# Performance work log

Hardware: AMD Instinct MI355X
Metric: run time of the kernel (lower is better)

## Reference

```python
import jax, jax.numpy as jnp
import numpy as np

B, T, S = 16, 512, 512
V, E, H = 10000, 512, 1024
L, K, MAXLEN = 6, 3, 1024
PAD_VAL = 1.0  # torch code pads conv input with tgt_pad_idx as a float value


def setup_inputs() -> dict:
    key = jax.random.key(0)
    ks = jax.random.split(key, 12)
    g = lambda k, shape: (jax.random.normal(k, shape, jnp.float32) * 0.02)
    return {
        "tgt": jax.random.randint(ks[0], (B, T), 0, V),
        "encoder_conved": jax.random.normal(ks[1], (B, S, E), jnp.float32),
        "encoder_combined": jax.random.normal(ks[2], (B, S, E), jnp.float32),
        "tok_emb": g(ks[3], (V, E)),
        "pos_emb": g(ks[4], (MAXLEN, E)),
        "emb2hid_w": g(ks[5], (E, H)), "emb2hid_b": jnp.zeros((H,), jnp.float32),
        "hid2emb_w": g(ks[6], (H, E)), "hid2emb_b": jnp.zeros((E,), jnp.float32),
        "attn_hid2emb_w": g(ks[7], (H, E)), "attn_hid2emb_b": jnp.zeros((E,), jnp.float32),
        "attn_emb2hid_w": g(ks[8], (E, H)), "attn_emb2hid_b": jnp.zeros((H,), jnp.float32),
        "fc_out_w": g(ks[9], (E, V)), "fc_out_b": jnp.zeros((V,), jnp.float32),
        "conv_w": g(ks[10], (L, 2 * H, H, K)),  # torch Conv1d weight: [out, in, k]
        "conv_b": jnp.zeros((L, 2 * H), jnp.float32),
    }


def reference(tgt, encoder_conved, encoder_combined, tok_emb, pos_emb,
              emb2hid_w, emb2hid_b, hid2emb_w, hid2emb_b,
              attn_hid2emb_w, attn_hid2emb_b, attn_emb2hid_w, attn_emb2hid_b,
              fc_out_w, fc_out_b, conv_w, conv_b):
    scale = jnp.float32(np.sqrt(0.5))
    b, t = tgt.shape
    h = emb2hid_w.shape[1]
    k = conv_w.shape[-1]

    # embeddings (dropout=0 -> identity)
    embedded = tok_emb[tgt] + pos_emb[jnp.arange(t)][None, :, :]   # [B,T,E]
    conv_input = (embedded @ emb2hid_w + emb2hid_b).transpose(0, 2, 1)  # [B,H,T]

    attention = None
    for l in range(conv_w.shape[0]):
        # causal left-pad with the (float) pad-index value, as in the torch code
        pad = jnp.full((b, h, k - 1), PAD_VAL, conv_input.dtype)
        x = jnp.concatenate([pad, conv_input], axis=2)              # [B,H,T+K-1]
        conved = jax.lax.conv_general_dilated(
            x, conv_w[l], window_strides=(1,), padding='VALID',
            dimension_numbers=('NCH', 'OIH', 'NCH')) + conv_b[l][None, :, None]  # [B,2H,T]
        a, g = jnp.split(conved, 2, axis=1)
        conved = a * jax.nn.sigmoid(g)                              # GLU -> [B,H,T]

        # single-head attention over encoder states
        conved_emb = conved.transpose(0, 2, 1) @ attn_hid2emb_w + attn_hid2emb_b  # [B,T,E]
        combined = (conved_emb + embedded) * scale
        energy = jnp.einsum('bte,bse->bts', combined, encoder_conved)
        attention = jax.nn.softmax(energy, axis=2)                  # [B,T,S]
        attended = jnp.einsum('bts,bse->bte', attention, encoder_combined)
        attended = attended @ attn_emb2hid_w + attn_emb2hid_b       # [B,T,H]
        conved = (conved + attended.transpose(0, 2, 1)) * scale     # [B,H,T]

        conv_input = (conved + conv_input) * scale                  # scaled residual

    conved = conv_input.transpose(0, 2, 1) @ hid2emb_w + hid2emb_b  # [B,T,E]
    output = conved @ fc_out_w + fc_out_b                           # [B,T,V]
    return output, attention
```

## Files before the change

kernel.cpp:

```cpp
#include <hip/hip_runtime.h>
#include <hip/hip_bf16.h>

typedef __attribute__((ext_vector_type(4))) float f32x4;
typedef __attribute__((ext_vector_type(8))) short short8;

#define DEVFN __device__ __forceinline__

static constexpr int Bn = 16, Tn = 512, Sn = 512, Vn = 10000, En = 512, Hn = 1024, Ln = 6;
static constexpr int Mn = Bn * Tn;
static constexpr int TP = Tn + 2;
static constexpr float kScale = 0.70710678118654752440f;

DEVFN float bf2f(__hip_bfloat16 x) { return __bfloat162float(x); }
DEVFN __hip_bfloat16 f2bf(float x) { return __float2bfloat16(x); }

struct bf16x4 { __hip_bfloat16 x, y, z, w; };

DEVFN void gload_lds16(const short* g, short* l) {
    __builtin_amdgcn_global_load_lds((const __attribute__((address_space(1))) void*)g,
                                     (__attribute__((address_space(3))) void*)l, 16, 0, 0);
}


__global__ void padfill_kernel(__hip_bfloat16* p) {
    p[threadIdx.x] = f2bf(1.0f);
}

__global__ void padrows_kernel(__hip_bfloat16* convinP) {
    int row = blockIdx.x;
    long base = ((long)(row >> 1) * TP + (row & 1)) * Hn;
    int e = threadIdx.x * 4;
    bf16x4 v{f2bf(1.f), f2bf(1.f), f2bf(1.f), f2bf(1.f)};
    *(bf16x4*)(convinP + base + e) = v;
}

__global__ void embed_kernel(const int* __restrict__ tgt, const float* __restrict__ tok,
                             const float* __restrict__ pos, const float* __restrict__ bah,
                             __hip_bfloat16* __restrict__ out, __hip_bfloat16* __restrict__ outA) {
    int row = blockIdx.x;
    int t = row & (Tn - 1);
    int v = tgt[row];
    const float* tr = tok + (long)v * En;
    const float* pr = pos + (long)t * En;
    int e = threadIdx.x * 4;
    float4 a = *(const float4*)(tr + e);
    float4 b = *(const float4*)(pr + e);
    float4 bb = *(const float4*)(bah + e);
    bf16x4 o{f2bf(a.x + b.x), f2bf(a.y + b.y), f2bf(a.z + b.z), f2bf(a.w + b.w)};
    *(bf16x4*)(out + (long)row * En + e) = o;
    bf16x4 oa{f2bf(kScale * (a.x + b.x + bb.x)), f2bf(kScale * (a.y + b.y + bb.y)),
              f2bf(kScale * (a.z + b.z + bb.z)), f2bf(kScale * (a.w + b.w + bb.w))};
    *(bf16x4*)(outA + (long)row * En + e) = oa;
}

__global__ void transpose_f32_bf16(const float* __restrict__ src, __hip_bfloat16* __restrict__ dst,
                                   int R, int C, long sZi, long sZo) {
    __shared__ float tile[32][33];
    src += (long)blockIdx.z * sZi;
    dst += (long)blockIdx.z * sZo;
    int c0 = blockIdx.x * 32, r0 = blockIdx.y * 32;
    for (int i = threadIdx.y; i < 32; i += 8) {
        int r = r0 + i, c = c0 + threadIdx.x;
        tile[i][threadIdx.x] = (r < R && c < C) ? src[(long)r * C + c] : 0.f;
    }
    __syncthreads();
    for (int i = threadIdx.y; i < 32; i += 8) {
        int c = c0 + i, r = r0 + threadIdx.x;
        if (c < C && r < R) dst[(long)c * R + r] = f2bf(tile[threadIdx.x][i]);
    }
}

__global__ void convert_bf16_kernel(const float* __restrict__ src, __hip_bfloat16* __restrict__ dst,
                                    long n4) {
    long i = (long)blockIdx.x * blockDim.x + threadIdx.x;
    if (i >= n4) return;
    long j = i * 4;
    float4 v = *(const float4*)(src + j);
    bf16x4 o{f2bf(v.x), f2bf(v.y), f2bf(v.z), f2bf(v.w)};
    *(bf16x4*)(dst + j) = o;
}

__global__ __launch_bounds__(256) void wpack2_kernel(const float* __restrict__ convw,
                                                     __hip_bfloat16* __restrict__ wp, int l) {
    __shared__ float row[3 * Hn];
    int c = blockIdx.x;
    int grp = c >> 5, w = c & 31;
    int o = (w < 16) ? grp * 16 + w : Hn + grp * 16 + (w - 16);
    const float* src = convw + ((long)(l * 2 * Hn + o)) * (Hn * 3);
#pragma unroll
    for (int j = 0; j < 3; ++j) {
        int idx = (j * 256 + threadIdx.x) * 4;
        *(float4*)&row[idx] = *(const float4*)(src + idx);
    }
    __syncthreads();
    __hip_bfloat16* dst = wp + (long)c * (3 * Hn);
#pragma unroll
    for (int j = 0; j < 3; ++j) {
        int kk = (j * 256 + threadIdx.x) * 4;
        int tap = kk >> 10;
        int i = kk & (Hn - 1);
        bf16x4 v{f2bf(row[i * 3 + tap]), f2bf(row[(i + 1) * 3 + tap]),
                 f2bf(row[(i + 2) * 3 + tap]), f2bf(row[(i + 3) * 3 + tap])};
        *(bf16x4*)(dst + kk) = v;
    }
}

__global__ __launch_bounds__(256) void softmax_kernel(const float* __restrict__ energy,
                                                      float* __restrict__ attn_f32,
                                                      __hip_bfloat16* __restrict__ attn_bf) {
    int row = blockIdx.x;
    const float* e = energy + (long)row * Sn;
    int tid = threadIdx.x;
    float v0 = e[tid], v1 = e[tid + 256];
    float m = fmaxf(v0, v1);
    for (int off = 32; off; off >>= 1) m = fmaxf(m, __shfl_xor(m, off));
    __shared__ float redm[4];
    __shared__ float reds[4];
    int lane = tid & 63, w = tid >> 6;
    if (lane == 0) redm[w] = m;
    __syncthreads();
    m = fmaxf(fmaxf(redm[0], redm[1]), fmaxf(redm[2], redm[3]));
    float x0 = __expf(v0 - m), x1 = __expf(v1 - m);
    float s = x0 + x1;
    for (int off = 32; off; off >>= 1) s += __shfl_xor(s, off);
    if (lane == 0) reds[w] = s;
    __syncthreads();
    s = reds[0] + reds[1] + reds[2] + reds[3];
    float inv = 1.f / s;
    long base = (long)row * Sn;
    if (attn_f32) {
        attn_f32[base + tid] = x0 * inv;
        attn_f32[base + tid + 256] = x1 * inv;
    }
    attn_bf[base + tid] = f2bf(x0 * inv);
    attn_bf[base + tid + 256] = f2bf(x1 * inv);
}

template <int EPI, bool OUTF32, bool NBOUND>
__global__ __launch_bounds__(256) void gemm_bf16(
    const __hip_bfloat16* __restrict__ A, const __hip_bfloat16* __restrict__ Bw,
    const float* __restrict__ bias, void* __restrict__ Cout,
    const __hip_bfloat16* __restrict__ R1, const __hip_bfloat16* __restrict__ R2,
    const float* __restrict__ R1f, const __hip_bfloat16* __restrict__ padrow,
    int M, int N, int K, long aZ, long bZ, long cZ, long r1Z, float s1, float s2) {
    __shared__ alignas(16) short As[2][128 * 32];
    __shared__ alignas(16) short Bs[2][128 * 32];
    const int tid = threadIdx.x;
    const int lane = tid & 63;
    const int wid = tid >> 6;
    const int wr = wid >> 1, wc = wid & 1;
    const int m0 = blockIdx.y * 128, n0 = blockIdx.x * 128;
    const short* Ag = (const short*)A + (long)blockIdx.z * aZ;
    const short* Bg = (const short*)Bw + (long)blockIdx.z * bZ;
    const short* pad = (const short*)padrow;

    f32x4 acc[4][4] = {};

    const int rc = tid >> 2;
    const int k8 = (tid & 3) * 8;

    auto stage = [&](int buf, int k0) {
#pragma unroll
        for (int j = 0; j < 2; ++j) {
            int r = rc + j * 64;
            const short* asrc = Ag + (long)(m0 + r) * K + k0 + k8;
            gload_lds16(asrc, &As[buf][r * 32 + k8]);
            int n = n0 + r;
            const short* bsrc = (NBOUND && n >= N) ? (pad + k8) : (Bg + (long)n * K + k0 + k8);
            gload_lds16(bsrc, &Bs[buf][r * 32 + k8]);
        }
    };

    const int rsel = lane & 15, hi = (lane >> 4) * 8;

    stage(0, 0);
    const int NT = K >> 5;
    for (int t = 0; t < NT; ++t) {
        const int cur = t & 1;
        if (t + 1 < NT) {
            stage(cur ^ 1, (t + 1) * 32);
            asm volatile("s_waitcnt vmcnt(4)" ::: "memory");
        } else {
            asm volatile("s_waitcnt vmcnt(0)" ::: "memory");
        }
        __builtin_amdgcn_s_barrier();
        __builtin_amdgcn_sched_barrier(0);
        short8 af[4], bg[4];
#pragma unroll
        for (int mi = 0; mi < 4; ++mi)
            af[mi] = *(const short8*)&As[cur][(wr * 64 + mi * 16 + rsel) * 32 + hi];
#pragma unroll
        for (int ni = 0; ni < 4; ++ni)
            bg[ni] = *(const short8*)&Bs[cur][(wc * 64 + ni * 16 + rsel) * 32 + hi];
        __builtin_amdgcn_s_setprio(1);
#pragma unroll
        for (int mi = 0; mi < 4; ++mi)
#pragma unroll
            for (int ni = 0; ni < 4; ++ni)
                acc[mi][ni] = __builtin_amdgcn_mfma_f32_16x16x32_bf16(af[mi], bg[ni], acc[mi][ni], 0, 0, 0);
        __builtin_amdgcn_s_setprio(0);
        __builtin_amdgcn_s_barrier();
        __builtin_amdgcn_sched_barrier(0);
    }

    const int rg = (lane >> 4) * 4;
    float* Cf = (float*)Cout + (long)blockIdx.z * cZ;
    __hip_bfloat16* Cb = (__hip_bfloat16*)Cout + (long)blockIdx.z * cZ;
    const __hip_bfloat16* R1z = R1 + (long)blockIdx.z * r1Z;
    const __hip_bfloat16* R2z = R2 + (long)blockIdx.z * cZ;
    const float* R1fz = R1f + (long)blockIdx.z * r1Z;
#pragma unroll
    for (int ni = 0; ni < 4; ++ni) {
        int col = n0 + wc * 64 + ni * 16 + rsel;
        if (NBOUND && col >= N) continue;
        float bi = (EPI != 3 && bias) ? bias[col] : 0.f;
#pragma unroll
        for (int mi = 0; mi < 4; ++mi) {
            int row = m0 + wr * 64 + mi * 16 + rg;
            f32x4 v = acc[mi][ni];
#pragma unroll
            for (int q = 0; q < 4; ++q) {
                long idx = (long)(row + q) * N + col;
                float x;
                if (EPI == 3) x = v[q] * s1 + R1fz[idx];
                else {
                    x = v[q] + bi;
                    if (EPI >= 1) x = (x + bf2f(R1z[idx])) * s1;
                    if (EPI >= 2) x = (x + bf2f(R2z[idx])) * s2;
                }
                if (OUTF32) Cf[idx] = x;
                else Cb[idx] = f2bf(x);
            }
        }
    }
}

template <int EPI, bool OUTF32>
__global__ __launch_bounds__(256) void gemm64(
    const __hip_bfloat16* __restrict__ A, const __hip_bfloat16* __restrict__ Bw,
    const float* __restrict__ bias, void* __restrict__ Cout,
    const __hip_bfloat16* __restrict__ R1, const __hip_bfloat16* __restrict__ R2,
    const float* __restrict__ R1f,
    int N, int K, long aZ, long bZ, long cZ, long r1Z, float s1, float s2) {
    __shared__ alignas(16) short As[2][64 * 32];
    __shared__ alignas(16) short Bs[2][128 * 32];
    const int tid = threadIdx.x;
    const int lane = tid & 63;
    const int wid = tid >> 6;
    const int m0 = blockIdx.y * 64, n0 = blockIdx.x * 128;
    const short* Ag = (const short*)A + (long)blockIdx.z * aZ;
    const short* Bg = (const short*)Bw + (long)blockIdx.z * bZ;

    f32x4 acc[4][2] = {};

    const int rc = tid >> 2;
    const int k8 = (tid & 3) * 8;

    auto stage = [&](int buf, int k0) {
        gload_lds16(Ag + (long)(m0 + rc) * K + k0 + k8, &As[buf][rc * 32 + k8]);
#pragma unroll
        for (int j = 0; j < 2; ++j) {
            int r = j * 64 + rc;
            gload_lds16(Bg + (long)(n0 + r) * K + k0 + k8, &Bs[buf][r * 32 + k8]);
        }
    };

    const int rsel = lane & 15, hi = (lane >> 4) * 8;

    stage(0, 0);
    const int NT = K >> 5;
    for (int t = 0; t < NT; ++t) {
        const int cur = t & 1;
        if (t + 1 < NT) {
            stage(cur ^ 1, (t + 1) * 32);
            asm volatile("s_waitcnt vmcnt(3)" ::: "memory");
        } else {
            asm volatile("s_waitcnt vmcnt(0)" ::: "memory");
        }
        __builtin_amdgcn_s_barrier();
        __builtin_amdgcn_sched_barrier(0);
        short8 af[4], bg[2];
#pragma unroll
        for (int mi = 0; mi < 4; ++mi)
            af[mi] = *(const short8*)&As[cur][(mi * 16 + rsel) * 32 + hi];
#pragma unroll
        for (int ni = 0; ni < 2; ++ni)
            bg[ni] = *(const short8*)&Bs[cur][(wid * 32 + ni * 16 + rsel) * 32 + hi];
        __builtin_amdgcn_s_setprio(1);
#pragma unroll
        for (int mi = 0; mi < 4; ++mi)
#pragma unroll
            for (int ni = 0; ni < 2; ++ni)
                acc[mi][ni] = __builtin_amdgcn_mfma_f32_16x16x32_bf16(af[mi], bg[ni], acc[mi][ni], 0, 0, 0);
        __builtin_amdgcn_s_setprio(0);
        __builtin_amdgcn_s_barrier();
        __builtin_amdgcn_sched_barrier(0);
    }

    const int rg = (lane >> 4) * 4;
    float* Cf = (float*)Cout + (long)blockIdx.z * cZ;
    __hip_bfloat16* Cb = (__hip_bfloat16*)Cout + (long)blockIdx.z * cZ;
    const __hip_bfloat16* R1z = R1 + (long)blockIdx.z * r1Z;
    const __hip_bfloat16* R2z = R2 + (long)blockIdx.z * cZ;
    const float* R1fz = R1f + (long)blockIdx.z * r1Z;
#pragma unroll
    for (int ni = 0; ni < 2; ++ni) {
        int col = n0 + wid * 32 + ni * 16 + rsel;
        float bi = (EPI != 3 && bias) ? bias[col] : 0.f;
#pragma unroll
        for (int mi = 0; mi < 4; ++mi) {
            int row = m0 + mi * 16 + rg;
            f32x4 v = acc[mi][ni];
#pragma unroll
            for (int q = 0; q < 4; ++q) {
                long idx = (long)(row + q) * N + col;
                float x;
                if (EPI == 3) x = v[q] * s1 + R1fz[idx];
                else {
                    x = v[q] + bi;
                    if (EPI >= 1) x = (x + bf2f(R1z[idx])) * s1;
                    if (EPI >= 2) x = (x + bf2f(R2z[idx])) * s2;
                }
                if (OUTF32) Cf[idx] = x;
                else Cb[idx] = f2bf(x);
            }
        }
    }
}

__global__ __launch_bounds__(512) void conv_glu_kernel(
    const __hip_bfloat16* __restrict__ Ain,
    const __hip_bfloat16* __restrict__ Bw,
    const float* __restrict__ bias, __hip_bfloat16* __restrict__ Cout,
    const __hip_bfloat16* __restrict__ padrow) {
    __shared__ alignas(16) short As[2][384 * 32];
    __shared__ alignas(16) short Bs[2][3 * 256 * 32];
    const int tid = threadIdx.x;
    const int lane = tid & 63;
    const int wid = tid >> 6;
    const int wr = wid >> 2, wc = wid & 3;
    const int n0 = blockIdx.x * 256, m0 = blockIdx.y * 256;
    const short* Ag = (const short*)Ain;
    const short* Bg = (const short*)Bw;
    const short* pad = (const short*)padrow;
    const int p0 = (m0 >> 9) * TP + 2 + (m0 & 511);

    f32x4 acc[8][4] = {};

    const int srow = tid >> 2;
    const int skey = (tid >> 3) & 3;
    const int scol = ((tid & 3) ^ skey) * 8;
    const int sdst = tid * 8;

    auto stageA = [&](int buf, int kt) {
        const int k0 = kt * 32;
#pragma unroll
        for (int j = 0; j < 3; ++j) {
            int prow = p0 - 128 + j * 128 + srow;
            const short* src = (prow >= 0) ? (Ag + (long)prow * Hn + k0 + scol) : (pad + scol);
            gload_lds16(src, &As[buf][j * 4096 + sdst]);
        }
    };
    auto stageB = [&](int buf, int kt) {
        const int k0 = kt * 32;
#pragma unroll
        for (int tap = 0; tap < 3; ++tap)
#pragma unroll
            for (int j = 0; j < 2; ++j) {
                int row = j * 128 + srow;
                const short* src = Bg + (long)(n0 + row) * 3072 + tap * 1024 + k0 + scol;
                gload_lds16(src, &Bs[buf][tap * 8192 + j * 4096 + sdst]);
            }
    };

    const int rsel = lane & 15, hi = (lane >> 4) * 8;

    stageA(0, 0); stageB(0, 0);
    for (int t = 0; t < 32; ++t) {
        const int cur = t & 1;
        if (t + 1 < 32) {
            stageA(cur ^ 1, t + 1); stageB(cur ^ 1, t + 1);
            asm volatile("s_waitcnt vmcnt(9)" ::: "memory");
        } else {
            asm volatile("s_waitcnt vmcnt(0)" ::: "memory");
        }
        __builtin_amdgcn_s_barrier();
        __builtin_amdgcn_sched_barrier(0);
#pragma unroll
        for (int tap = 0; tap < 3; ++tap) {
            short8 bg[4];
#pragma unroll
            for (int ni = 0; ni < 4; ++ni) {
                int row = wc * 64 + ni * 16 + rsel;
                int xk = ((row >> 1) & 3) << 3;
                bg[ni] = *(const short8*)&Bs[cur][tap * 8192 + row * 32 + (hi ^ xk)];
            }
#pragma unroll
            for (int mh = 0; mh < 2; ++mh) {
                short8 af[4];
#pragma unroll
                for (int i = 0; i < 4; ++i) {
                    int row = 126 + tap + wr * 128 + mh * 64 + i * 16 + rsel;
                    int xk = ((row >> 1) & 3) << 3;
                    af[i] = *(const short8*)&As[cur][row * 32 + (hi ^ xk)];
                }
                __builtin_amdgcn_s_setprio(1);
#pragma unroll
                for (int i = 0; i < 4; ++i)
#pragma unroll
                    for (int ni = 0; ni < 4; ++ni)
                        acc[mh * 4 + i][ni] = __builtin_amdgcn_mfma_f32_16x16x32_bf16(
                            af[i], bg[ni], acc[mh * 4 + i][ni], 0, 0, 0);
                __builtin_amdgcn_s_setprio(0);
                __builtin_amdgcn_sched_barrier(0);
            }
        }
        __builtin_amdgcn_s_barrier();
        __builtin_amdgcn_sched_barrier(0);
    }

    const int rg = (lane >> 4) * 4;
    const int No = Hn;
#pragma unroll
    for (int p = 0; p < 2; ++p) {
        int jcol = ((n0 + wc * 64) >> 1) + p * 16 + rsel;
        float ba = bias[jcol];
        float bgv = bias[Hn + jcol];
#pragma unroll
        for (int mi = 0; mi < 8; ++mi) {
            int row = m0 + wr * 128 + mi * 16 + rg;
            f32x4 va = acc[mi][2 * p], vg = acc[mi][2 * p + 1];
#pragma unroll
            for (int q = 0; q < 4; ++q) {
                float a = va[q] + ba;
                float g = vg[q] + bgv;
                Cout[(long)(row + q) * No + jcol] = f2bf(a * (1.f / (1.f + __expf(-g))));
            }
        }
    }
}

template <bool OUTF32, bool NBOUND>
__global__ __launch_bounds__(512) void gemm256(
    const __hip_bfloat16* __restrict__ A, const __hip_bfloat16* __restrict__ Bw,
    const float* __restrict__ bias, void* __restrict__ Cout,
    const __hip_bfloat16* __restrict__ padrow, int M, int N, int K) {
    __shared__ alignas(16) short As[2][256 * 64];
    __shared__ alignas(16) short Bs[2][256 * 64];
    const int tid = threadIdx.x;
    const int lane = tid & 63;
    const int wid = tid >> 6;
    const int wr = wid >> 2, wc = wid & 3;
    const int n0 = blockIdx.x * 256, m0 = blockIdx.y * 256;
    const short* Ag = (const short*)A;
    const short* Bg = (const short*)Bw;
    const short* pad = (const short*)padrow;

    f32x4 acc[8][4] = {};

    const int srow_l = tid >> 3;
    const int scol = ((tid & 7) ^ (srow_l & 7)) * 8;
    const int sdst = (tid >> 3) * 64 + (tid & 7) * 8;

    auto stage = [&](int buf, int kt) {
        const int k0 = kt * 64;
#pragma unroll
        for (int j = 0; j < 4; ++j) {
            const int row = j * 64 + srow_l;
            const short* asrc = Ag + (long)(m0 + row) * K + k0 + scol;
            gload_lds16(asrc, &As[buf][j * 4096 + sdst]);
            int n = n0 + row;
            const short* bsrc = (NBOUND && n >= N) ? (pad + scol) : (Bg + (long)n * K + k0 + scol);
            gload_lds16(bsrc, &Bs[buf][j * 4096 + sdst]);
        }
    };

    const int rsel = lane & 15, hi = (lane >> 4) * 8;
    const int xorc = (rsel & 7) << 3;

    stage(0, 0);
    const int NT = K >> 6;
    for (int t = 0; t < NT; ++t) {
        const int cur = t & 1;
        if (t + 1 < NT) {
            stage(cur ^ 1, t + 1);
            asm volatile("s_waitcnt vmcnt(8)" ::: "memory");
        } else {
            asm volatile("s_waitcnt vmcnt(0)" ::: "memory");
        }
        __builtin_amdgcn_s_barrier();
        __builtin_amdgcn_sched_barrier(0);
        short8 bg[2][2][2];
#pragma unroll
        for (int nh = 0; nh < 2; ++nh)
#pragma unroll
            for (int i = 0; i < 2; ++i) {
                const int row = wc * 64 + nh * 32 + i * 16 + rsel;
#pragma unroll
                for (int ks = 0; ks < 2; ++ks)
                    bg[nh][i][ks] = *(const short8*)&Bs[cur][row * 64 + ((ks * 32 + hi) ^ xorc)];
            }
#pragma unroll
        for (int mh = 0; mh < 2; ++mh) {
            short8 af[4][2];
#pragma unroll
            for (int i = 0; i < 4; ++i) {
                const int row = wr * 128 + mh * 64 + i * 16 + rsel;
#pragma unroll
                for (int ks = 0; ks < 2; ++ks)
                    af[i][ks] = *(const short8*)&As[cur][row * 64 + ((ks * 32 + hi) ^ xorc)];
            }
            __builtin_amdgcn_s_setprio(1);
#pragma unroll
            for (int nh = 0; nh < 2; ++nh)
#pragma unroll
                for (int i = 0; i < 4; ++i)
#pragma unroll
                    for (int jn = 0; jn < 2; ++jn)
#pragma unroll
                        for (int ks = 0; ks < 2; ++ks)
                            acc[mh * 4 + i][nh * 2 + jn] = __builtin_amdgcn_mfma_f32_16x16x32_bf16(
                                af[i][ks], bg[nh][jn][ks], acc[mh * 4 + i][nh * 2 + jn], 0, 0, 0);
            __builtin_amdgcn_s_setprio(0);
            __builtin_amdgcn_sched_barrier(0);
        }
        __builtin_amdgcn_s_barrier();
        __builtin_amdgcn_sched_barrier(0);
    }

    const int rg = (lane >> 4) * 4;
    float* Cf = (float*)Cout;
    __hip_bfloat16* Cb = (__hip_bfloat16*)Cout;
#pragma unroll
    for (int ni = 0; ni < 4; ++ni) {
        int col = n0 + wc * 64 + ni * 16 + rsel;
        if (NBOUND && col >= N) continue;
        float bi = bias ? bias[col] : 0.f;
#pragma unroll
        for (int mi = 0; mi < 8; ++mi) {
            int row = m0 + wr * 128 + mi * 16 + rg;
            f32x4 v = acc[mi][ni];
#pragma unroll
            for (int q = 0; q < 4; ++q) {
                long idx = (long)(row + q) * N + col;
                float x = v[q] + bi;
                if (OUTF32) Cf[idx] = x;
                else Cb[idx] = f2bf(x);
            }
        }
    }
}


extern "C" void kernel_launch(void* const* d_in, const int* in_sizes, int n_in,
                              void* d_out, int out_size, void* d_ws, size_t ws_size,
                              hipStream_t stream) {
    const int* tgt = (const int*)d_in[0];
    const float* enc_conved = (const float*)d_in[1];
    const float* enc_combined = (const float*)d_in[2];
    const float* tok_emb = (const float*)d_in[3];
    const float* pos_emb = (const float*)d_in[4];
    const float* w_e2h = (const float*)d_in[5];
    const float* b_e2h = (const float*)d_in[6];
    const float* w_h2e = (const float*)d_in[7];
    const float* b_h2e = (const float*)d_in[8];
    const float* w_ah2e = (const float*)d_in[9];
    const float* b_ah2e = (const float*)d_in[10];
    const float* w_ae2h = (const float*)d_in[11];
    const float* b_ae2h = (const float*)d_in[12];
    const float* w_fc = (const float*)d_in[13];
    const float* b_fc = (const float*)d_in[14];
    const float* conv_w = (const float*)d_in[15];
    const float* conv_b = (const float*)d_in[16];

    char* ws = (char*)d_ws;
    size_t off = 0;
    auto alloc = [&](size_t bytes) { size_t r = off; off = (off + bytes + 255) & ~(size_t)255; return r; };
    __hip_bfloat16* emb    = (__hip_bfloat16*)(ws + alloc((size_t)Mn * En * 2));
    __hip_bfloat16* embA   = (__hip_bfloat16*)(ws + alloc((size_t)Mn * En * 2));
    __hip_bfloat16* convinP= (__hip_bfloat16*)(ws + alloc((size_t)Bn * TP * Hn * 2));
    __hip_bfloat16* conved = (__hip_bfloat16*)(ws + alloc((size_t)Mn * Hn * 2));
    size_t o_en = alloc((size_t)Mn * Sn * 4);
    float* energy = (float*)(ws + o_en);
    __hip_bfloat16* encm = (__hip_bfloat16*)(ws + o_en);
    __hip_bfloat16* attnbf = (__hip_bfloat16*)(ws + alloc((size_t)Mn * Sn * 2));
    __hip_bfloat16* wT_e2h = (__hip_bfloat16*)(ws + alloc((size_t)Hn * En * 2));
    __hip_bfloat16* wT_h2e = (__hip_bfloat16*)(ws + alloc((size_t)En * Hn * 2));
    __hip_bfloat16* wT_ae2h= (__hip_bfloat16*)(ws + alloc((size_t)Hn * En * 2));
    __hip_bfloat16* wbAH   = (__hip_bfloat16*)(ws + alloc((size_t)Hn * En * 2));
    __hip_bfloat16* wT_fc  = (__hip_bfloat16*)(ws + alloc((size_t)Vn * En * 2));
    __hip_bfloat16* encc   = (__hip_bfloat16*)(ws + alloc((size_t)Bn * Sn * En * 2));
    __hip_bfloat16* encAH  = (__hip_bfloat16*)(ws + alloc((size_t)Bn * Sn * Hn * 2));
    __hip_bfloat16* encCW  = (__hip_bfloat16*)(ws + alloc((size_t)Bn * Hn * Sn * 2));
    float* embE            = (float*)(ws + alloc((size_t)Mn * Sn * 4));
    __hip_bfloat16* padrow = (__hip_bfloat16*)(ws + alloc(256));
    __hip_bfloat16* wpack  = (__hip_bfloat16*)(ws + alloc((size_t)2 * Hn * 3 * Hn * 2));
    __hip_bfloat16* tmpE = conved;
    __hip_bfloat16* convinD = convinP + 2 * Hn;

    float* out = (float*)d_out;
    float* attn_out = out + (long)Mn * Vn;
    const long bSq = (long)Sn * Sn;
    const long bSH = (long)Sn * Hn;
    const long bTH = (long)Tn * Hn;
    const long bTE = (long)Tn * En;
    const long bPH = (long)TP * Hn;

    dim3 tb(32, 8);
    const __hip_bfloat16* nb = nullptr;
    const float* nf = nullptr;

    padfill_kernel<<<1, 128, 0, stream>>>(padrow);
    padrows_kernel<<<2 * Bn, 256, 0, stream>>>(convinP);
    embed_kernel<<<Mn, 128, 0, stream>>>(tgt, tok_emb, pos_emb, b_ah2e, emb, embA);
    transpose_f32_bf16<<<dim3(Hn / 32, En / 32, 1), tb, 0, stream>>>(w_e2h, wT_e2h, En, Hn, 0, 0);
    transpose_f32_bf16<<<dim3(En / 32, Hn / 32, 1), tb, 0, stream>>>(w_h2e, wT_h2e, Hn, En, 0, 0);
    transpose_f32_bf16<<<dim3(Hn / 32, En / 32, 1), tb, 0, stream>>>(w_ae2h, wT_ae2h, En, Hn, 0, 0);
    transpose_f32_bf16<<<dim3((Vn + 31) / 32, En / 32, 1), tb, 0, stream>>>(w_fc, wT_fc, En, Vn, 0, 0);
    convert_bf16_kernel<<<((long)Hn * En / 4 + 255) / 256, 256, 0, stream>>>(w_ah2e, wbAH, (long)Hn * En / 4);
    convert_bf16_kernel<<<((long)Bn * Sn * En / 4 + 255) / 256, 256, 0, stream>>>(enc_conved, encc, (long)Bn * Sn * En / 4);
    convert_bf16_kernel<<<((long)Bn * Sn * En / 4 + 255) / 256, 256, 0, stream>>>(enc_combined, encm, (long)Bn * Sn * En / 4);

    gemm_bf16<0, false, false><<<dim3(Hn / 128, Sn / 128, Bn), 256, 0, stream>>>(
        encc, wbAH, nullptr, encAH, nb, nb, nf, padrow, Sn, Hn, En, bSq, 0, bSH, 0, 1.f, 1.f);
    gemm_bf16<0, false, false><<<dim3(Sn / 128, Hn / 128, Bn), 256, 0, stream>>>(
        wT_ae2h, encm, nullptr, encCW, nb, nb, nf, padrow, Hn, Sn, En, 0, bSq, bSH, 0, 1.f, 1.f);
    gemm64<0, true><<<dim3(Sn / 128, Tn / 64, Bn), 256, 0, stream>>>(
        embA, encc, nullptr, embE, nb, nb, nf, Sn, En, bTE, bSq, bSq, 0, 1.f, 1.f);
    gemm_bf16<0, false, false><<<dim3(Hn / 128, Tn / 128, Bn), 256, 0, stream>>>(
        emb, wT_e2h, b_e2h, convinD, nb, nb, nf, padrow, Tn, Hn, En, bTE, 0, bPH, 0, 1.f, 1.f);

    for (int l = 0; l < Ln; ++l) {
        wpack2_kernel<<<2 * Hn, 256, 0, stream>>>(conv_w, wpack, l);
        conv_glu_kernel<<<dim3(2 * Hn / 256, Mn / 256), 512, 0, stream>>>(
            convinP, wpack, conv_b + (long)l * 2 * Hn, conved, padrow);
        gemm64<3, true><<<dim3(Sn / 128, Tn / 64, Bn), 256, 0, stream>>>(
            conved, encAH, nullptr, energy, nb, nb, embE, Sn, Hn, bTH, bSH, bSq, bSq, kScale, 1.f);
        softmax_kernel<<<Mn, 256, 0, stream>>>(energy, (l == Ln - 1) ? attn_out : nullptr, attnbf);
        gemm_bf16<2, false, false><<<dim3(Hn / 128, Tn / 128, Bn), 256, 0, stream>>>(
            attnbf, encCW, b_ae2h, convinD, conved, convinD, nf, padrow,
            Tn, Hn, Sn, bSq, bSH, bPH, bTH, kScale, kScale);
    }

    gemm64<0, false><<<dim3(En / 128, Tn / 64, Bn), 256, 0, stream>>>(
        convinD, wT_h2e, b_h2e, tmpE, nb, nb, nf, En, Hn, bPH, 0, bTE, 0, 1.f, 1.f);
    gemm256<true, true><<<dim3((Vn + 255) / 256, Mn / 256), 512, 0, stream>>>(
        tmpE, wT_fc, b_fc, out, padrow, Mn, Vn, En);
}
```

Baseline: 1.243 ms.

## Retile conv-GLU kernel to full-sequence row tiles with two-row halo

The causal conv kernel now assigns each block one full 512-step sequence (plus a 2-row causal halo) by 128 output channels, instead of 256x256 tiles. The old tiles loaded a 128-row halo for every 256 output rows. The new shape loads only 2 extra rows, because the halo comes straight from the pre-padded input buffer. This drops the separate pad-row pointer and shrinks the weight tile. Per-wave wait counts are adjusted for the uneven number of async loads. The aim is less global-to-LDS traffic per output and smaller shared memory, at the cost of relying on the padded input layout and asymmetric waitcnt logic.

New measurement: 1.222 ms. Within noise of the previous version (-1.8%).

```diff
diff --git a/kernel.cpp b/kernel.cpp
--- a/kernel.cpp
+++ b/kernel.cpp
@@ -331,19 +331,18 @@
 __global__ __launch_bounds__(512) void conv_glu_kernel(
     const __hip_bfloat16* __restrict__ Ain,
     const __hip_bfloat16* __restrict__ Bw,
-    const float* __restrict__ bias, __hip_bfloat16* __restrict__ Cout,
-    const __hip_bfloat16* __restrict__ padrow) {
-    __shared__ alignas(16) short As[2][384 * 32];
-    __shared__ alignas(16) short Bs[2][3 * 256 * 32];
+    const float* __restrict__ bias, __hip_bfloat16* __restrict__ Cout) {
+    __shared__ alignas(16) short As[2][516 * 32];
+    __shared__ alignas(16) short Bs[2][3 * 128 * 32];
     const int tid = threadIdx.x;
     const int lane = tid & 63;
     const int wid = tid >> 6;
-    const int wr = wid >> 2, wc = wid & 3;
-    const int n0 = blockIdx.x * 256, m0 = blockIdx.y * 256;
+    const int wr = wid >> 1, wc = wid & 1;
+    const int n0 = blockIdx.x * 128;
+    const int m0 = blockIdx.y * 512;
+    const int seqbase = blockIdx.y * TP;
     const short* Ag = (const short*)Ain;
     const short* Bg = (const short*)Bw;
-    const short* pad = (const short*)padrow;
-    const int p0 = (m0 >> 9) * TP + 2 + (m0 & 511);
 
     f32x4 acc[8][4] = {};
 
@@ -355,22 +354,22 @@
     auto stageA = [&](int buf, int kt) {
         const int k0 = kt * 32;
 #pragma unroll
-        for (int j = 0; j < 3; ++j) {
-            int prow = p0 - 128 + j * 128 + srow;
-            const short* src = (prow >= 0) ? (Ag + (long)prow * Hn + k0 + scol) : (pad + scol);
-            gload_lds16(src, &As[buf][j * 4096 + sdst]);
+        for (int j = 0; j < 4; ++j) {
+            int r = j * 128 + srow;
+            gload_lds16(Ag + (long)(seqbase + r) * Hn + k0 + scol, &As[buf][j * 4096 + sdst]);
+        }
+        if (tid < 8) {
+            int r = 512 + (tid >> 2);
+            gload_lds16(Ag + (long)(seqbase + r) * Hn + k0 + (tid & 3) * 8,
+                        &As[buf][4 * 4096 + sdst]);
         }
     };
     auto stageB = [&](int buf, int kt) {
         const int k0 = kt * 32;
 #pragma unroll
         for (int tap = 0; tap < 3; ++tap)
-#pragma unroll
-            for (int j = 0; j < 2; ++j) {
-                int row = j * 128 + srow;
-                const short* src = Bg + (long)(n0 + row) * 3072 + tap * 1024 + k0 + scol;
-                gload_lds16(src, &Bs[buf][tap * 8192 + j * 4096 + sdst]);
-            }
+            gload_lds16(Bg + (long)(n0 + srow) * 3072 + tap * 1024 + k0 + scol,
+                        &Bs[buf][tap * 4096 + sdst]);
     };
 
     const int rsel = lane & 15, hi = (lane >> 4) * 8;
@@ -380,7 +379,8 @@
         const int cur = t & 1;
         if (t + 1 < 32) {
             stageA(cur ^ 1, t + 1); stageB(cur ^ 1, t + 1);
-            asm volatile("s_waitcnt vmcnt(9)" ::: "memory");
+            if (wid == 0) asm volatile("s_waitcnt vmcnt(8)" ::: "memory");
+            else          asm volatile("s_waitcnt vmcnt(7)" ::: "memory");
         } else {
             asm volatile("s_waitcnt vmcnt(0)" ::: "memory");
         }
@@ -393,14 +393,14 @@
             for (int ni = 0; ni < 4; ++ni) {
                 int row = wc * 64 + ni * 16 + rsel;
                 int xk = ((row >> 1) & 3) << 3;
-                bg[ni] = *(const short8*)&Bs[cur][tap * 8192 + row * 32 + (hi ^ xk)];
+                bg[ni] = *(const short8*)&Bs[cur][tap * 4096 + row * 32 + (hi ^ xk)];
             }
 #pragma unroll
             for (int mh = 0; mh < 2; ++mh) {
                 short8 af[4];
 #pragma unroll
                 for (int i = 0; i < 4; ++i) {
-                    int row = 126 + tap + wr * 128 + mh * 64 + i * 16 + rsel;
+                    int row = wr * 128 + mh * 64 + i * 16 + rsel + tap;
                     int xk = ((row >> 1) & 3) << 3;
                     af[i] = *(const short8*)&As[cur][row * 32 + (hi ^ xk)];
                 }
@@ -632,8 +632,8 @@
 
     for (int l = 0; l < Ln; ++l) {
         wpack2_kernel<<<2 * Hn, 256, 0, stream>>>(conv_w, wpack, l);
-        conv_glu_kernel<<<dim3(2 * Hn / 256, Mn / 256), 512, 0, stream>>>(
-            convinP, wpack, conv_b + (long)l * 2 * Hn, conved, padrow);
+        conv_glu_kernel<<<dim3(2 * Hn / 128, Mn / 512), 512, 0, stream>>>(
+            convinP, wpack, conv_b + (long)l * 2 * Hn, conved);
         gemm64<3, true><<<dim3(Sn / 128, Tn / 64, Bn), 256, 0, stream>>>(
             conved, encAH, nullptr, energy, nb, nb, embE, Sn, Hn, bTH, bSH, bSq, bSq, kScale, 1.f);
         softmax_kernel<<<Mn, 256, 0, stream>>>(energy, (l == Ln - 1) ? attn_out : nullptr, attnbf);
```
